# Kernel tuning notes

Hardware: AMD Instinct MI355X
Metric: run time of the kernel (lower is better)

## Reference

```python
import jax, jax.numpy as jnp
import numpy as np

B, N, D_MODEL, H = 2, 2048, 1024, 16
HD = D_MODEL // H  # head_dim = 64

def setup_inputs() -> dict:
    key = jax.random.key(0)
    ks = jax.random.split(key, 5)
    x = jax.random.normal(ks[0], (B, N, D_MODEL), dtype=jnp.float32)
    scale = 0.02
    # Linear weights stored as [in, out] (torch does x @ W.T with W [out,in]; equivalent math)
    Wq = jax.random.normal(ks[1], (D_MODEL, D_MODEL), dtype=jnp.float32) * scale
    Wk = jax.random.normal(ks[2], (D_MODEL, D_MODEL), dtype=jnp.float32) * scale
    Wv = jax.random.normal(ks[3], (D_MODEL, D_MODEL), dtype=jnp.float32) * scale
    Wo = jax.random.normal(ks[4], (D_MODEL, D_MODEL), dtype=jnp.float32) * scale
    return {"x": x, "Wq": Wq, "Wk": Wk, "Wv": Wv, "Wo": Wo}

def reference(x, Wq, Wk, Wv, Wo):
    b, n, _ = x.shape
    # QKV projections (no bias; qkv_bias=False)
    q = (x @ Wq).reshape(b, n, H, HD)
    k = (x @ Wk).reshape(b, n, H, HD)
    v = (x @ Wv).reshape(b, n, H, HD)
    # scores [b, h, q, k]
    scores = jnp.einsum('bqhd,bkhd->bhqk', q, k) / jnp.sqrt(jnp.float32(HD))
    causal = jnp.triu(jnp.ones((n, n), dtype=bool), k=1)  # True above diagonal -> masked
    scores = jnp.where(causal, -jnp.inf, scores)
    attn = jax.nn.softmax(scores, axis=-1)  # dropout p=0.0 -> identity
    ctx = jnp.einsum('bhqk,bkhd->bqhd', attn, v).reshape(b, n, D_MODEL)
    return ctx @ Wo
```

## Files before the change

kernel.cpp:

```cpp
#include <hip/hip_runtime.h>
#include <math.h>

#define D_MODEL 1024
#define NHEAD 16
#define HD 64
#define SEQ 2048
#define BATCH 2
#define MTOT (BATCH * SEQ)

typedef __attribute__((ext_vector_type(8))) short bf16x8;
typedef __attribute__((ext_vector_type(4))) float f32x4;

__device__ __forceinline__ unsigned short f2bf(float f) {
    unsigned int u = __float_as_uint(f);
    u += 0x7FFF + ((u >> 16) & 1);
    return (unsigned short)(u >> 16);
}

__device__ __forceinline__ unsigned int pk2bf(float a, float b) {
    unsigned int r;
    asm("v_cvt_pk_bf16_f32 %0, %1, %2" : "=v"(r) : "v"(a), "v"(b));
    return r;
}

__device__ __forceinline__ void async16(unsigned short* lds, const unsigned short* g) {
    __builtin_amdgcn_global_load_lds(
        (const __attribute__((address_space(1))) unsigned int*)g,
        (__attribute__((address_space(3))) unsigned int*)lds, 16, 0, 0);
}

__device__ __forceinline__ void BAR() {
    asm volatile("" ::: "memory");
    __builtin_amdgcn_s_barrier();
    asm volatile("" ::: "memory");
}

__global__ __launch_bounds__(256) void prep(const float* __restrict__ x,
                                            unsigned short* __restrict__ xb,
                                            const float* __restrict__ W0,
                                            const float* __restrict__ W1,
                                            const float* __restrict__ W2,
                                            const float* __restrict__ W3,
                                            unsigned short* __restrict__ Wt) {
    const int bid = blockIdx.x;
    const int tid = threadIdx.x;
    if (bid < 4096) {
        const int i = (bid * 256 + tid) * 4;
        float4 v = *(const float4*)(x + i);
        uint2 pk;
        pk.x = pk2bf(v.x, v.y);
        pk.y = pk2bf(v.z, v.w);
        *(uint2*)(xb + i) = pk;
    } else {
        __shared__ float T[32][33];
        const int t = bid - 4096;
        const int z = t >> 10, rem = t & 1023;
        const int n0 = (rem & 31) * 32, k0 = (rem >> 5) * 32;
        const float* W = (z == 0) ? W0 : (z == 1) ? W1 : (z == 2) ? W2 : W3;
        unsigned short* out = Wt + (size_t)z * D_MODEL * D_MODEL;
        const int tx = tid & 31, ty = tid >> 5;
#pragma unroll
        for (int i = 0; i < 4; ++i)
            T[ty + 8 * i][tx] = W[(size_t)(k0 + ty + 8 * i) * D_MODEL + n0 + tx];
        __syncthreads();
#pragma unroll
        for (int i = 0; i < 4; ++i)
            out[(size_t)(n0 + ty + 8 * i) * D_MODEL + k0 + tx] = f2bf(T[tx][ty + 8 * i]);
    }
}

__global__ __launch_bounds__(512, 2) void qkv_mfma(const unsigned short* __restrict__ A,
                                                   const unsigned short* __restrict__ Wt,
                                                   unsigned short* __restrict__ q,
                                                   unsigned short* __restrict__ k,
                                                   unsigned short* __restrict__ vt) {
    __shared__ unsigned short SM[65536];
    const int tid = threadIdx.x;
    const int wave = tid >> 6, lane = tid & 63;
    const int quad = lane >> 4, l16 = lane & 15;
    const int wm = wave >> 2, wn = wave & 3;

    const int bid = blockIdx.x;
    const int swz = (bid & 7) * 24 + (bid >> 3);
    const int by = swz / 12, bx = swz % 12;
    const int m0 = by * 256;
    const int z = bx >> 2, c0 = (bx & 3) * 256;
    const unsigned short* Bz = Wt + (size_t)z * D_MODEL * D_MODEL;

    const unsigned short* aptr[2];
    const unsigned short* bptr[2];
    int ldsoff[2];
#pragma unroll
    for (int j = 0; j < 2; ++j) {
        const int s = j * 512 + tid;
        const int r = s >> 2;
        const int cg = (s & 3) ^ ((r + (r >> 2)) & 3);
        aptr[j] = A + (size_t)(m0 + r) * D_MODEL + cg * 8;
        bptr[j] = Bz + (size_t)(c0 + r) * D_MODEL + cg * 8;
        ldsoff[j] = (j * 512 + wave * 64) * 8;
    }

    const int key = (l16 + (l16 >> 2)) & 3;
    const int chunk = quad ^ key;
    int aoff[8], boff[4];
#pragma unroll
    for (int mt = 0; mt < 8; ++mt)
        aoff[mt] = ((wm * 128 + mt * 16 + l16) * 4 + chunk) * 8;
#pragma unroll
    for (int nt = 0; nt < 4; ++nt)
        boff[nt] = 16384 + ((wn * 64 + nt * 16 + l16) * 4 + chunk) * 8;

    f32x4 acc[8][4];
#pragma unroll
    for (int mt = 0; mt < 8; ++mt)
#pragma unroll
        for (int nt = 0; nt < 4; ++nt)
            acc[mt][nt] = (f32x4){0.f, 0.f, 0.f, 0.f};

    auto stage = [&](int d, int op, int ks, int T) {
        const int base = d * 32768 + op * 16384 + ks * 8192;
#pragma unroll
        for (int j = 0; j < 2; ++j)
            async16(SM + base + ldsoff[j],
                    (op ? bptr[j] : aptr[j]) + T * 64 + ks * 32);
    };
    auto dsA = [&](bf16x8* af, int mh, int d, int ks) {
        const int base = d * 32768 + ks * 8192;
#pragma unroll
        for (int i = 0; i < 4; ++i)
            af[i] = *(const bf16x8*)&SM[base + aoff[mh * 4 + i]];
    };
    auto dsB = [&](bf16x8* bf, int d, int ks) {
        const int base = d * 32768 + ks * 8192;
#pragma unroll
        for (int i = 0; i < 4; ++i)
            bf[i] = *(const bf16x8*)&SM[base + boff[i]];
    };
    auto mfma16 = [&](bf16x8* af, bf16x8* bf, int mh) {
        __builtin_amdgcn_s_setprio(1);
#pragma unroll
        for (int i = 0; i < 4; ++i)
#pragma unroll
            for (int nt = 0; nt < 4; ++nt)
                acc[mh * 4 + i][nt] = __builtin_amdgcn_mfma_f32_16x16x32_bf16(
                    af[i], bf[nt], acc[mh * 4 + i][nt], 0, 0, 0);
        __builtin_amdgcn_s_setprio(0);
    };

    stage(0, 0, 0, 0);
    stage(0, 1, 0, 0);
    stage(0, 0, 1, 0);
    stage(0, 1, 1, 0);
    asm volatile("s_waitcnt vmcnt(4)" ::: "memory");
    BAR();

    const int NT = D_MODEL / 64;
    for (int T = 0; T < NT; ++T) {
        const int d = T & 1, dn = d ^ 1;
        const bool nx = (T + 1 < NT);
        bf16x8 af[4], bf[4];
        if (nx) stage(dn, 0, 0, T + 1);
        dsA(af, 0, d, 0);
        dsB(bf, d, 0);
        mfma16(af, bf, 0);
        BAR();
        if (nx) stage(dn, 1, 0, T + 1);
        dsA(af, 1, d, 0);
        mfma16(af, bf, 1);
        if (nx) asm volatile("s_waitcnt vmcnt(4)" ::: "memory");
        else    asm volatile("s_waitcnt vmcnt(0)" ::: "memory");
        BAR();
        if (nx) stage(dn, 0, 1, T + 1);
        dsA(af, 0, d, 1);
        dsB(bf, d, 1);
        mfma16(af, bf, 0);
        BAR();
        if (nx) stage(dn, 1, 1, T + 1);
        dsA(af, 1, d, 1);
        mfma16(af, bf, 1);
        if (nx) asm volatile("s_waitcnt vmcnt(4)" ::: "memory");
        else    asm volatile("s_waitcnt vmcnt(0)" ::: "memory");
        BAR();
    }

    __syncthreads();
    const int bb = m0 >> 11, tok0 = m0 & (SEQ - 1), h0 = c0 >> 6;
    if (z < 2) {
        const float qsc = (z == 0) ? 0.18033688011112042f : 1.0f;
        unsigned short* dst = (z == 0) ? q : k;
#pragma unroll
        for (int pass = 0; pass < 2; ++pass) {
            if (pass) __syncthreads();
            if (wm == pass) {
#pragma unroll
                for (int mt = 0; mt < 8; ++mt)
#pragma unroll
                    for (int nt = 0; nt < 4; ++nt)
#pragma unroll
                        for (int reg = 0; reg < 4; ++reg) {
                            const int rr = mt * 16 + quad * 4 + reg;
                            const int cc = wn * 64 + nt * 16 + l16;
                            SM[rr * 264 + cc] = f2bf(acc[mt][nt][reg] * qsc);
                        }
            }
            __syncthreads();
#pragma unroll
            for (int it = 0; it < 8; ++it) {
                const int g = it * 512 + tid;
                const int r = g >> 5, gg = g & 31;
                uint4 val = *(const uint4*)&SM[r * 264 + gg * 8];
                *(uint4*)(dst + (((size_t)bb * NHEAD + h0 + (gg >> 3)) * SEQ +
                                 tok0 + pass * 128 + r) * HD + (gg & 7) * 8) = val;
            }
        }
    } else {
#pragma unroll
        for (int pass = 0; pass < 2; ++pass) {
            if (pass) __syncthreads();
            if (wm == pass) {
#pragma unroll
                for (int mt = 0; mt < 8; ++mt)
#pragma unroll
                    for (int nt = 0; nt < 4; ++nt) {
                        const int dd = wn * 64 + nt * 16 + l16;
                        const int m = mt * 16 + quad * 4;
                        uint2 w;
                        w.x = pk2bf(acc[mt][nt][0], acc[mt][nt][1]);
                        w.y = pk2bf(acc[mt][nt][2], acc[mt][nt][3]);
                        *(uint2*)&SM[dd * 136 + m] = w;
                    }
            }
            __syncthreads();
#pragma unroll
            for (int it = 0; it < 8; ++it) {
                const int g = it * 512 + tid;
                const int dd = g >> 4, tg = (g & 15) * 8;
                uint4 val = *(const uint4*)&SM[dd * 136 + tg];
                *(uint4*)(vt + (((size_t)bb * NHEAD + h0 + (dd >> 6)) * HD + (dd & 63)) * SEQ +
                          tok0 + pass * 128 + tg) = val;
            }
        }
    }
}

__global__ __launch_bounds__(256) void gemm_out(const unsigned short* __restrict__ A,
                                                const unsigned short* __restrict__ Bw,
                                                float* __restrict__ outf) {
    __shared__ unsigned short SM[16384];
    const int tid = threadIdx.x;
    const int m0 = blockIdx.y * 128, n0 = blockIdx.x * 128;
    const int wave = tid >> 6, lane = tid & 63;
    const int quad = lane >> 4, l16 = lane & 15;
    const int wm = wave & 1, wn = wave >> 1;

    f32x4 acc[4][4];
#pragma unroll
    for (int mt = 0; mt < 4; ++mt)
#pragma unroll
        for (int nt = 0; nt < 4; ++nt)
            acc[mt][nt] = (f32x4){0.f, 0.f, 0.f, 0.f};

    for (int k0 = 0; k0 < D_MODEL; k0 += 64) {
        __syncthreads();
#pragma unroll
        for (int i = 0; i < 4; ++i) {
            const int c = i * 256 + tid;
            const int r = c >> 3, cc = (c & 7) * 8;
            const int cbase = i * 256 + wave * 64;
            async16(SM + cbase * 8, A + (size_t)(m0 + r) * D_MODEL + k0 + cc);
            async16(SM + 8192 + cbase * 8, Bw + (size_t)(n0 + r) * D_MODEL + k0 + cc);
        }
        __syncthreads();
#pragma unroll
        for (int ks = 0; ks < 2; ++ks) {
            bf16x8 af[4], bfr[4];
#pragma unroll
            for (int mt = 0; mt < 4; ++mt)
                af[mt] = *(const bf16x8*)&SM[(wm * 64 + mt * 16 + l16) * 64 + ks * 32 + quad * 8];
#pragma unroll
            for (int nt = 0; nt < 4; ++nt)
                bfr[nt] = *(const bf16x8*)&SM[8192 + (wn * 64 + nt * 16 + l16) * 64 + ks * 32 + quad * 8];
#pragma unroll
            for (int mt = 0; mt < 4; ++mt)
#pragma unroll
                for (int nt = 0; nt < 4; ++nt)
                    acc[mt][nt] = __builtin_amdgcn_mfma_f32_16x16x32_bf16(
                        af[mt], bfr[nt], acc[mt][nt], 0, 0, 0);
        }
    }

#pragma unroll
    for (int mt = 0; mt < 4; ++mt)
#pragma unroll
        for (int nt = 0; nt < 4; ++nt)
#pragma unroll
            for (int reg = 0; reg < 4; ++reg) {
                const int m = m0 + wm * 64 + mt * 16 + quad * 4 + reg;
                const int n = n0 + wn * 64 + nt * 16 + l16;
                outf[(size_t)m * D_MODEL + n] = acc[mt][nt][reg];
            }
}

__global__ __launch_bounds__(256, 2) void attn_mfma(const unsigned short* __restrict__ Q,
                                                    const unsigned short* __restrict__ K,
                                                    const unsigned short* __restrict__ VT,
                                                    unsigned short* __restrict__ ctx) {
    __shared__ float CMB[8832];
    const int tid = threadIdx.x;
    const int wave = tid >> 6, lane = tid & 63;
    const int quad = lane >> 4, l16 = lane & 15;
    const int h = blockIdx.x, b = blockIdx.z;
    const int y = blockIdx.y;
    const unsigned short* Qp = Q + ((size_t)b * NHEAD + h) * SEQ * HD;
    const unsigned short* Kp = K + ((size_t)b * NHEAD + h) * SEQ * HD;
    const unsigned short* Vp = VT + ((size_t)b * NHEAD + h) * HD * SEQ;
    unsigned short* Pw = (unsigned short*)CMB + wave * 4096;
    const int sw8 = l16 & 7;

#pragma unroll 1
    for (int half = 0; half < 2; ++half) {
        const int p = half ? y : (31 - y);
        const int row0 = p * 64;
        if (half) __syncthreads();

        bf16x8 bQ[4][2];
#pragma unroll
        for (int f = 0; f < 4; ++f)
#pragma unroll
            for (int ks = 0; ks < 2; ++ks)
                bQ[f][ks] = *(const bf16x8*)(Qp +
                    (size_t)(row0 + f * 16 + l16) * HD + ks * 32 + quad * 8);

        f32x4 o[4][4];
        float ps[4] = {0.f, 0.f, 0.f, 0.f};
#pragma unroll
        for (int nt = 0; nt < 4; ++nt)
#pragma unroll
            for (int f = 0; f < 4; ++f)
                o[nt][f] = (f32x4){0.f, 0.f, 0.f, 0.f};

        for (int kt = wave; kt <= p; kt += 4) {
            bf16x8 aK[4][2], aV[4][2];
#pragma unroll
            for (int mt = 0; mt < 4; ++mt)
#pragma unroll
                for (int ks = 0; ks < 2; ++ks)
                    aK[mt][ks] = *(const bf16x8*)(Kp +
                        (size_t)(kt * 64 + mt * 16 + l16) * HD + ks * 32 + quad * 8);
#pragma unroll
            for (int nt = 0; nt < 4; ++nt)
#pragma unroll
                for (int ks = 0; ks < 2; ++ks)
                    aV[nt][ks] = *(const bf16x8*)(Vp +
                        (size_t)(nt * 16 + l16) * SEQ + kt * 64 + ks * 32 + quad * 8);

            f32x4 sT[4][4];
            __builtin_amdgcn_s_setprio(1);
#pragma unroll
            for (int mt = 0; mt < 4; ++mt)
#pragma unroll
                for (int f = 0; f < 4; ++f) {
                    sT[mt][f] = __builtin_amdgcn_mfma_f32_16x16x32_bf16(
                        aK[mt][0], bQ[f][0], (f32x4){0.f, 0.f, 0.f, 0.f}, 0, 0, 0);
                    sT[mt][f] = __builtin_amdgcn_mfma_f32_16x16x32_bf16(
                        aK[mt][1], bQ[f][1], sT[mt][f], 0, 0, 0);
                }
            __builtin_amdgcn_s_setprio(0);

            const bool diag = (kt == p);
#pragma unroll
            for (int mt = 0; mt < 4; ++mt)
#pragma unroll
                for (int f = 0; f < 4; ++f) {
                    float pv[4];
#pragma unroll
                    for (int reg = 0; reg < 4; ++reg)
                        pv[reg] = exp2f(sT[mt][f][reg]);
                    if (diag) {
                        const int kb = kt * 64 + mt * 16 + quad * 4;
                        const int qg = row0 + f * 16 + l16;
#pragma unroll
                        for (int reg = 0; reg < 4; ++reg)
                            pv[reg] = (kb + reg > qg) ? 0.f : pv[reg];
                    }
                    ps[f] += (pv[0] + pv[1]) + (pv[2] + pv[3]);
                    uint2 w;
                    w.x = pk2bf(pv[0], pv[1]);
                    w.y = pk2bf(pv[2], pv[3]);
                    const int gph = ((mt * 2 + (quad >> 1)) ^ sw8);
                    *(uint2*)&Pw[(f * 16 + l16) * 64 + gph * 8 + (quad & 1) * 4] = w;
                }

            bf16x8 bP[4][2];
#pragma unroll
            for (int f = 0; f < 4; ++f)
#pragma unroll
                for (int ks = 0; ks < 2; ++ks)
                    bP[f][ks] = *(const bf16x8*)&Pw[(f * 16 + l16) * 64 +
                                                    ((ks * 4 + quad) ^ sw8) * 8];

            __builtin_amdgcn_s_setprio(1);
#pragma unroll
            for (int nt = 0; nt < 4; ++nt)
#pragma unroll
                for (int f = 0; f < 4; ++f) {
                    o[nt][f] = __builtin_amdgcn_mfma_f32_16x16x32_bf16(
                        aV[nt][0], bP[f][0], o[nt][f], 0, 0, 0);
                    o[nt][f] = __builtin_amdgcn_mfma_f32_16x16x32_bf16(
                        aV[nt][1], bP[f][1], o[nt][f], 0, 0, 0);
                }
            __builtin_amdgcn_s_setprio(0);
        }

#pragma unroll
        for (int f = 0; f < 4; ++f) {
            ps[f] += __shfl_xor(ps[f], 16);
            ps[f] += __shfl_xor(ps[f], 32);
        }

        __syncthreads();
        if (wave >= 2) {
            float* Rg = CMB + (wave - 2) * 4352;
#pragma unroll
            for (int nt = 0; nt < 4; ++nt)
#pragma unroll
                for (int f = 0; f < 4; ++f)
                    *(f32x4*)&Rg[(f * 16 + l16) * 68 + nt * 16 + quad * 4] = o[nt][f];
            if (quad == 0)
#pragma unroll
                for (int f = 0; f < 4; ++f)
                    CMB[8704 + (wave - 2) * 64 + f * 16 + l16] = ps[f];
        }
        __syncthreads();
        if (wave < 2) {
            float* Rg = CMB + wave * 4352;
#pragma unroll
            for (int nt = 0; nt < 4; ++nt)
#pragma unroll
                for (int f = 0; f < 4; ++f)
                    o[nt][f] += *(const f32x4*)&Rg[(f * 16 + l16) * 68 + nt * 16 + quad * 4];
#pragma unroll
            for (int f = 0; f < 4; ++f)
                ps[f] += CMB[8704 + wave * 64 + f * 16 + l16];
        }
        __syncthreads();
        if (wave == 1) {
#pragma unroll
            for (int nt = 0; nt < 4; ++nt)
#pragma unroll
                for (int f = 0; f < 4; ++f)
                    *(f32x4*)&CMB[(f * 16 + l16) * 68 + nt * 16 + quad * 4] = o[nt][f];
            if (quad == 0)
#pragma unroll
                for (int f = 0; f < 4; ++f)
                    CMB[8704 + f * 16 + l16] = ps[f];
        }
        __syncthreads();
        if (wave == 0) {
#pragma unroll
            for (int nt = 0; nt < 4; ++nt)
#pragma unroll
                for (int f = 0; f < 4; ++f)
                    o[nt][f] += *(const f32x4*)&CMB[(f * 16 + l16) * 68 + nt * 16 + quad * 4];
            float inv[4];
#pragma unroll
            for (int f = 0; f < 4; ++f)
                inv[f] = 1.f / (ps[f] + CMB[8704 + f * 16 + l16]);
#pragma unroll
            for (int nt = 0; nt < 4; ++nt)
#pragma unroll
                for (int f = 0; f < 4; ++f) {
                    const int tok = row0 + f * 16 + l16;
                    const int col = h * HD + nt * 16 + quad * 4;
                    uint2 w;
                    w.x = pk2bf(o[nt][f][0] * inv[f], o[nt][f][1] * inv[f]);
                    w.y = pk2bf(o[nt][f][2] * inv[f], o[nt][f][3] * inv[f]);
                    *(uint2*)(ctx + ((size_t)b * SEQ + tok) * D_MODEL + col) = w;
                }
        }
    }
}

extern "C" void kernel_launch(void* const* d_in, const int* in_sizes, int n_in,
                              void* d_out, int out_size, void* d_ws, size_t ws_size,
                              hipStream_t stream) {
    const float* x  = (const float*)d_in[0];
    const float* Wq = (const float*)d_in[1];
    const float* Wk = (const float*)d_in[2];
    const float* Wv = (const float*)d_in[3];
    const float* Wo = (const float*)d_in[4];
    float* out = (float*)d_out;

    unsigned short* ws = (unsigned short*)d_ws;
    const size_t T = (size_t)MTOT * D_MODEL;
    unsigned short* xb  = ws;
    unsigned short* Wt  = ws + T;
    unsigned short* q   = ws + 2 * T;
    unsigned short* k   = ws + 3 * T;
    unsigned short* vt  = ws + 4 * T;
    unsigned short* ctx = ws + 5 * T;

    prep<<<dim3(8192), dim3(256), 0, stream>>>(x, xb, Wq, Wk, Wv, Wo, Wt);

    qkv_mfma<<<dim3(192), dim3(512), 0, stream>>>(xb, Wt, q, k, vt);

    attn_mfma<<<dim3(NHEAD, 16, BATCH), dim3(256), 0, stream>>>(q, k, vt, ctx);

    gemm_out<<<dim3(8, 32), dim3(256), 0, stream>>>(ctx, Wt + 3 * (size_t)D_MODEL * D_MODEL, out);
}
```

Before: 189.0 us.

## Software-pipeline K tile loads with double-buffered registers in attention loop

Restructures the attention inner loop into a two-stage software pipeline. K fragments for the next tile are prefetched into a ping-pong register buffer while the current tile's QK^T MFMAs run, and the V loads are issued after the score MFMAs. It also switches exp2f to the raw hardware exp2 builtin. The extra register buffer raises VGPR pressure under launch_bounds(256,2), which could cause spills or lower occupancy.

```diff
diff --git a/kernel.cpp b/kernel.cpp
--- a/kernel.cpp
+++ b/kernel.cpp
@@ -301,6 +301,65 @@
             }
 }
 
+#define ATTN_ITER(CUR, NXT, KT, KTN)                                           \
+  do {                                                                         \
+    const int kt_ = (KT);                                                      \
+    const int ktn_ = (KTN);                                                    \
+    f32x4 sT[4][4];                                                            \
+    __builtin_amdgcn_s_setprio(1);                                             \
+    _Pragma("unroll") for (int mt = 0; mt < 4; ++mt)                           \
+        _Pragma("unroll") for (int f = 0; f < 4; ++f) {                        \
+      sT[mt][f] = __builtin_amdgcn_mfma_f32_16x16x32_bf16(                     \
+          CUR[mt][0], bQ[f][0], (f32x4){0.f, 0.f, 0.f, 0.f}, 0, 0, 0);         \
+      sT[mt][f] = __builtin_amdgcn_mfma_f32_16x16x32_bf16(                     \
+          CUR[mt][1], bQ[f][1], sT[mt][f], 0, 0, 0);                           \
+    }                                                                          \
+    __builtin_amdgcn_s_setprio(0);                                             \
+    if (ktn_ <= p) {           \
+      _Pragma("unroll") for (int mt = 0; mt < 4; ++mt)                         \
+          _Pragma("unroll") for (int ks = 0; ks < 2; ++ks)                     \
+        NXT[mt][ks] = *(const bf16x8*)(Kp +                                    \
+            (size_t)(ktn_ * 64 + mt * 16 + l16) * HD + ks * 32 + quad * 8);    \
+    }                                                                          \
+    _Pragma("unroll") for (int nt = 0; nt < 4; ++nt)  \
+        _Pragma("unroll") for (int ks = 0; ks < 2; ++ks)      \
+      aV[nt][ks] = *(const bf16x8*)(Vp +                                       \
+          (size_t)(nt * 16 + l16) * SEQ + kt_ * 64 + ks * 32 + quad * 8);      \
+    const bool diag = (kt_ == p);                                              \
+    _Pragma("unroll") for (int mt = 0; mt < 4; ++mt)                           \
+        _Pragma("unroll") for (int f = 0; f < 4; ++f) {                        \
+      float pv[4];                                                             \
+      _Pragma("unroll") for (int reg = 0; reg < 4; ++reg)                      \
+          pv[reg] = __builtin_amdgcn_exp2f(sT[mt][f][reg]);                    \
+      if (diag) {                                                              \
+        const int kb = kt_ * 64 + mt * 16 + quad * 4;                          \
+        const int qg = row0 + f * 16 + l16;                                    \
+        _Pragma("unroll") for (int reg = 0; reg < 4; ++reg)                    \
+            pv[reg] = (kb + reg > qg) ? 0.f : pv[reg];                         \
+      }                                                                        \
+      ps[f] += (pv[0] + pv[1]) + (pv[2] + pv[3]);                              \
+      uint2 w;                                                                 \
+      w.x = pk2bf(pv[0], pv[1]);                                               \
+      w.y = pk2bf(pv[2], pv[3]);                                               \
+      const int gph = ((mt * 2 + (quad >> 1)) ^ sw8);                          \
+      *(uint2*)&Pw[(f * 16 + l16) * 64 + gph * 8 + (quad & 1) * 4] = w;        \
+    }                                                                          \
+    bf16x8 bP[4][2];                                                           \
+    _Pragma("unroll") for (int f = 0; f < 4; ++f)                              \
+        _Pragma("unroll") for (int ks = 0; ks < 2; ++ks)                       \
+      bP[f][ks] = *(const bf16x8*)&Pw[(f * 16 + l16) * 64 +                    \
+                                      ((ks * 4 + quad) ^ sw8) * 8];            \
+    __builtin_amdgcn_s_setprio(1);                                             \
+    _Pragma("unroll") for (int nt = 0; nt < 4; ++nt)                           \
+        _Pragma("unroll") for (int f = 0; f < 4; ++f) {                        \
+      o[nt][f] = __builtin_amdgcn_mfma_f32_16x16x32_bf16(                      \
+          aV[nt][0], bP[f][0], o[nt][f], 0, 0, 0);                             \
+      o[nt][f] = __builtin_amdgcn_mfma_f32_16x16x32_bf16(                      \
+          aV[nt][1], bP[f][1], o[nt][f], 0, 0, 0);                             \
+    }                                                                          \
+    __builtin_amdgcn_s_setprio(0);                                             \
+  } while (0)
+
 __global__ __launch_bounds__(256, 2) void attn_mfma(const unsigned short* __restrict__ Q,
                                                     const unsigned short* __restrict__ K,
                                                     const unsigned short* __restrict__ VT,
@@ -339,77 +398,20 @@
             for (int f = 0; f < 4; ++f)
                 o[nt][f] = (f32x4){0.f, 0.f, 0.f, 0.f};
 
-        for (int kt = wave; kt <= p; kt += 4) {
-            bf16x8 aK[4][2], aV[4][2];
+        bf16x8 Ka[4][2], Kb[4][2], aV[4][2];
+        if (wave <= p) {
 #pragma unroll
             for (int mt = 0; mt < 4; ++mt)
 #pragma unroll
                 for (int ks = 0; ks < 2; ++ks)
-                    aK[mt][ks] = *(const bf16x8*)(Kp +
-                        (size_t)(kt * 64 + mt * 16 + l16) * HD + ks * 32 + quad * 8);
-#pragma unroll
-            for (int nt = 0; nt < 4; ++nt)
-#pragma unroll
-                for (int ks = 0; ks < 2; ++ks)
-                    aV[nt][ks] = *(const bf16x8*)(Vp +
-                        (size_t)(nt * 16 + l16) * SEQ + kt * 64 + ks * 32 + quad * 8);
-
-            f32x4 sT[4][4];
-            __builtin_amdgcn_s_setprio(1);
-#pragma unroll
-            for (int mt = 0; mt < 4; ++mt)
-#pragma unroll
-                for (int f = 0; f < 4; ++f) {
-                    sT[mt][f] = __builtin_amdgcn_mfma_f32_16x16x32_bf16(
-                        aK[mt][0], bQ[f][0], (f32x4){0.f, 0.f, 0.f, 0.f}, 0, 0, 0);
-                    sT[mt][f] = __builtin_amdgcn_mfma_f32_16x16x32_bf16(
-                        aK[mt][1], bQ[f][1], sT[mt][f], 0, 0, 0);
-                }
-            __builtin_amdgcn_s_setprio(0);
-
-            const bool diag = (kt == p);
-#pragma unroll
-            for (int mt = 0; mt < 4; ++mt)
-#pragma unroll
-                for (int f = 0; f < 4; ++f) {
-                    float pv[4];
-#pragma unroll
-                    for (int reg = 0; reg < 4; ++reg)
-                        pv[reg] = exp2f(sT[mt][f][reg]);
-                    if (diag) {
-                        const int kb = kt * 64 + mt * 16 + quad * 4;
-                        const int qg = row0 + f * 16 + l16;
-#pragma unroll
-                        for (int reg = 0; reg < 4; ++reg)
-                            pv[reg] = (kb + reg > qg) ? 0.f : pv[reg];
-                    }
-                    ps[f] += (pv[0] + pv[1]) + (pv[2] + pv[3]);
-                    uint2 w;
-                    w.x = pk2bf(pv[0], pv[1]);
-                    w.y = pk2bf(pv[2], pv[3]);
-                    const int gph = ((mt * 2 + (quad >> 1)) ^ sw8);
-                    *(uint2*)&Pw[(f * 16 + l16) * 64 + gph * 8 + (quad & 1) * 4] = w;
-                }
-
-            bf16x8 bP[4][2];
-#pragma unroll
-            for (int f = 0; f < 4; ++f)
-#pragma unroll
-                for (int ks = 0; ks < 2; ++ks)
-                    bP[f][ks] = *(const bf16x8*)&Pw[(f * 16 + l16) * 64 +
-                                                    ((ks * 4 + quad) ^ sw8) * 8];
-
-            __builtin_amdgcn_s_setprio(1);
-#pragma unroll
-            for (int nt = 0; nt < 4; ++nt)
-#pragma unroll
-                for (int f = 0; f < 4; ++f) {
-                    o[nt][f] = __builtin_amdgcn_mfma_f32_16x16x32_bf16(
-                        aV[nt][0], bP[f][0], o[nt][f], 0, 0, 0);
-                    o[nt][f] = __builtin_amdgcn_mfma_f32_16x16x32_bf16(
-                        aV[nt][1], bP[f][1], o[nt][f], 0, 0, 0);
-                }
-            __builtin_amdgcn_s_setprio(0);
+                    Ka[mt][ks] = *(const bf16x8*)(Kp +
+                        (size_t)(wave * 64 + mt * 16 + l16) * HD + ks * 32 + quad * 8);
+        }
+
+#pragma unroll 1
+        for (int kt = wave; kt <= p; kt += 8) {
+            ATTN_ITER(Ka, Kb, kt, kt + 4);
+            if (kt + 4 <= p) ATTN_ITER(Kb, Ka, kt + 4, kt + 8);
         }
 
 #pragma unroll
```

Result: slower. 217.4 us (+15.0%).
